# Kernel optimization log

Hardware: AMD Instinct MI355X
Metric: run time of the kernel (lower is better)

## Reference

```python
import math
import jax, jax.numpy as jnp
import numpy as np

BATCH, DEPTH = 16, 12
N_NODES = 2 ** DEPTH - 1  # 4095, heap layout: children of i are 2i+1, 2i+2
IN_F, OUT_F, STATE_F = 512, 512, 256


def setup_inputs() -> dict:
    key = jax.random.key(0)
    ks = jax.random.split(key, 10)
    x_batch = jax.random.normal(ks[0], (BATCH, N_NODES, IN_F), dtype=jnp.float32)
    idx_batch = jnp.arange(BATCH, dtype=jnp.int32)
    W_in = jax.random.normal(ks[1], (IN_F, IN_F), dtype=jnp.float32) / math.sqrt(IN_F)
    b_in = jnp.zeros((IN_F,), dtype=jnp.float32)
    u1 = jax.random.uniform(ks[2], (STATE_F,), dtype=jnp.float32)
    u2 = jax.random.uniform(ks[3], (STATE_F,), dtype=jnp.float32)
    nu_log = jnp.log(-0.5 * jnp.log(u1 + 1e-6))
    theta_log = jnp.log(2.0 * math.pi * u2)
    lam_mod = jnp.exp(-jnp.exp(nu_log))
    gamma_log = jnp.log(jnp.sqrt(1.0 - jnp.square(lam_mod)))
    B_re = jax.random.normal(ks[4], (STATE_F, IN_F), dtype=jnp.float32) / math.sqrt(2 * IN_F)
    B_im = jax.random.normal(ks[5], (STATE_F, IN_F), dtype=jnp.float32) / math.sqrt(2 * IN_F)
    C_re = jax.random.normal(ks[6], (OUT_F, STATE_F), dtype=jnp.float32) / math.sqrt(STATE_F)
    C_im = jax.random.normal(ks[7], (OUT_F, STATE_F), dtype=jnp.float32) / math.sqrt(STATE_F)
    return dict(x_batch=x_batch, idx_batch=idx_batch, W_in=W_in, b_in=b_in,
                nu_log=nu_log, theta_log=theta_log, gamma_log=gamma_log,
                B_re=B_re, B_im=B_im, C_re=C_re, C_im=C_im)


def reference(x_batch, idx_batch, W_in, b_in, nu_log, theta_log, gamma_log,
              B_re, B_im, C_re, C_im):
    bsz, n_nodes, _ = x_batch.shape
    depth = int(round(math.log2(n_nodes + 1)))
    S = B_re.shape[0]

    # LRU constants (complex lambda kept as (re, im) pair)
    lam_mod = jnp.exp(-jnp.exp(nu_log))           # [S]
    th = jnp.exp(theta_log)
    lr, li = lam_mod * jnp.cos(th), lam_mod * jnp.sin(th)
    gamma = jnp.exp(gamma_log)                    # [S]

    proj = x_batch @ W_in.T + b_in                # [B, N, IN]
    # complex input term (proj is real): proj @ B^T
    in_re = jnp.einsum('bni,si->bns', proj, B_re) # [B, N, S]
    in_im = jnp.einsum('bni,si->bns', proj, B_im)

    h_re = jnp.zeros((bsz, n_nodes, S), dtype=proj.dtype)
    h_im = jnp.zeros((bsz, n_nodes, S), dtype=proj.dtype)

    # process levels bottom-up; level d nodes occupy [2^d-1, 2^{d+1}-1)
    for d in range(depth - 1, -1, -1):
        a, b = 2 ** d - 1, 2 ** (d + 1) - 1
        n = b - a
        if d == depth - 1:  # leaves: left/right = -1 -> zero child state
            cr = jnp.zeros((bsz, n, S), dtype=proj.dtype)
            ci = jnp.zeros((bsz, n, S), dtype=proj.dtype)
        else:
            # children of nodes [a, b) are the contiguous block [2a+1, 2b+1)
            cr = h_re[:, 2 * a + 1:2 * b + 1].reshape(bsz, n, 2, S).sum(axis=2)
            ci = h_im[:, 2 * a + 1:2 * b + 1].reshape(bsz, n, 2, S).sum(axis=2)
        hr = lr * cr - li * ci + gamma * in_re[:, a:b]
        hi = lr * ci + li * cr + gamma * in_im[:, a:b]
        h_re = h_re.at[:, a:b].set(hr)
        h_im = h_im.at[:, a:b].set(hi)

    # y = Re(h @ C^T), computed once on final states (same math as per-level scatter)
    outputs = jnp.einsum('bns,os->bno', h_re, C_re) - jnp.einsum('bns,os->bno', h_im, C_im)
    return outputs
```

## Files before the change

kernel.cpp:

```cpp
#include <hip/hip_runtime.h>


#define ROWS 65520
#define KDIM 512

typedef __attribute__((ext_vector_type(8))) short bf16x8;
typedef __attribute__((ext_vector_type(4))) float f32x4;

__device__ __forceinline__ unsigned short f2bf(float f) {
    unsigned int u = __float_as_uint(f);
    unsigned int r = (u + 0x7FFFu + ((u >> 16) & 1u)) >> 16;
    return (unsigned short)r;
}
__device__ __forceinline__ float b2f(unsigned short h) {
    return __uint_as_float(((unsigned int)h) << 16);
}

__global__ __launch_bounds__(256) void cvt_f32_bf16(const float* __restrict__ in,
                                                    unsigned short* __restrict__ out,
                                                    int n4) {
    int i = blockIdx.x * 256 + threadIdx.x;
    if (i < n4) {
        float4 v = ((const float4*)in)[i];
        ushort4 o;
        o.x = f2bf(v.x); o.y = f2bf(v.y); o.z = f2bf(v.z); o.w = f2bf(v.w);
        ((ushort4*)out)[i] = o;
    }
}

__global__ __launch_bounds__(256) void prep_M(const float* __restrict__ W,
                                              const float* __restrict__ Bre,
                                              const float* __restrict__ Bim,
                                              const float* __restrict__ gamma_log,
                                              unsigned short* __restrict__ M16) {
    __shared__ float Bs[16][17];
    __shared__ float Ws[16][17];
    int tx = threadIdx.x, ty = threadIdx.y;
    int j  = blockIdx.x * 16 + tx;
    int cc = blockIdx.y * 16 + ty;
    const float* Bsel = (cc < 256) ? (Bre + (size_t)cc * 512)
                                   : (Bim + (size_t)(cc - 256) * 512);
    float acc = 0.f;
    for (int kt = 0; kt < 512; kt += 16) {
        Bs[ty][tx] = Bsel[kt + tx];
        Ws[ty][tx] = W[(size_t)(kt + ty) * 512 + j];
        __syncthreads();
#pragma unroll
        for (int k = 0; k < 16; ++k) acc += Bs[ty][k] * Ws[k][tx];
        __syncthreads();
    }
    float g = expf(gamma_log[cc & 255]);
    M16[(size_t)cc * 512 + j] = f2bf(acc * g);
}

__global__ __launch_bounds__(64) void prep_bias(const float* __restrict__ bin,
                                                const float* __restrict__ Bre,
                                                const float* __restrict__ Bim,
                                                const float* __restrict__ gamma_log,
                                                float* __restrict__ biasc) {
    const int c = blockIdx.x;
    const int t = threadIdx.x;
    const float* Bsel = (c < 256) ? (Bre + (size_t)c * 512)
                                  : (Bim + (size_t)(c - 256) * 512);
    float acc = 0.f;
#pragma unroll
    for (int i = t; i < 512; i += 64) acc += bin[i] * Bsel[i];
#pragma unroll
    for (int off = 32; off > 0; off >>= 1) acc += __shfl_down(acc, off, 64);
    if (t == 0) biasc[c] = acc * expf(gamma_log[c & 255]);
}

__global__ __launch_bounds__(256) void prep_C(const float* __restrict__ Cre,
                                              const float* __restrict__ Cim,
                                              unsigned short* __restrict__ C16) {
    int idx = blockIdx.x * 256 + threadIdx.x;
    int o = idx >> 9;
    int s = idx & 511;
    float v = (s < 256) ? Cre[(size_t)o * 256 + s] : -Cim[(size_t)o * 256 + (s - 256)];
    C16[idx] = f2bf(v);
}

template <bool OUT_BF16>
__global__ __launch_bounds__(256) void gemm_mfma(const unsigned short* __restrict__ A,
                                                 const unsigned short* __restrict__ Bm,
                                                 const float* __restrict__ bias,
                                                 void* __restrict__ Cout,
                                                 int Mrows) {
    __shared__ __align__(16) unsigned short As[128 * 64];
    __shared__ __align__(16) unsigned short Bs[128 * 64];
    const int t = threadIdx.x;
    const int lane = t & 63;
    const int w = t >> 6;
    const int wr = (w >> 1) * 64;
    const int wc = (w & 1) * 64;
    const int bid = blockIdx.x;
    const int xcd = bid & 7;
    const int lid = bid >> 3;
    const int rowblk = xcd * 64 + (lid >> 2);
    const int colblk = lid & 3;
    const int row0 = rowblk * 128;
    const int col0 = colblk * 128;
    const int kt0  = (rowblk & 7) * 64;

    f32x4 acc[4][4] = {};

    for (int it = 0; it < 8; ++it) {
        const int kt = (kt0 + it * 64) & 511;
#pragma unroll
        for (int q = 0; q < 4; ++q) {
            int c   = q * 256 + t;
            int row = c >> 3;
            int kc  = c & 7;
            int kg  = kc ^ (row & 7);
            int ar  = row0 + row; if (ar >= Mrows) ar = Mrows - 1;
            const unsigned short* ga = A + (size_t)ar * KDIM + kt + kg * 8;
            __builtin_amdgcn_global_load_lds(
                (const __attribute__((address_space(1))) unsigned int*)ga,
                (__attribute__((address_space(3))) unsigned int*)(As + c * 8),
                16, 0, 0);
            const unsigned short* gb = Bm + (size_t)(col0 + row) * KDIM + kt + kg * 8;
            __builtin_amdgcn_global_load_lds(
                (const __attribute__((address_space(1))) unsigned int*)gb,
                (__attribute__((address_space(3))) unsigned int*)(Bs + c * 8),
                16, 0, 0);
        }
        __syncthreads();
#pragma unroll
        for (int kk = 0; kk < 64; kk += 32) {
            const int kgc = kk >> 3;
            bf16x8 af[4], bfr[4];
#pragma unroll
            for (int i = 0; i < 4; ++i) {
                int row = wr + i * 16 + (lane & 15);
                int kca = (kgc + (lane >> 4)) ^ (row & 7);
                af[i] = *(const bf16x8*)(As + row * 64 + kca * 8);
                int colr = wc + i * 16 + (lane & 15);
                int kcb = (kgc + (lane >> 4)) ^ (colr & 7);
                bfr[i] = *(const bf16x8*)(Bs + colr * 64 + kcb * 8);
            }
#pragma unroll
            for (int i = 0; i < 4; ++i)
#pragma unroll
                for (int j = 0; j < 4; ++j)
                    acc[i][j] = __builtin_amdgcn_mfma_f32_16x16x32_bf16(
                        af[i], bfr[j], acc[i][j], 0, 0, 0);
        }
        __syncthreads();
    }

    const int cq = lane >> 4;
    const int cl = lane & 15;
#pragma unroll
    for (int i = 0; i < 4; ++i) {
#pragma unroll
        for (int j = 0; j < 4; ++j) {
#pragma unroll
            for (int r = 0; r < 4; ++r) {
                int grow = row0 + wr + i * 16 + cq * 4 + r;
                int gcol = col0 + wc + j * 16 + cl;
                if (grow < Mrows) {
                    float v = acc[i][j][r];
                    if (bias) v += bias[gcol];
                    if (OUT_BF16)
                        ((unsigned short*)Cout)[(size_t)grow * 512 + gcol] = f2bf(v);
                    else
                        ((float*)Cout)[(size_t)grow * 512 + gcol] = v;
                }
            }
        }
    }
}

template <int E>
__global__ __launch_bounds__(256) void tree_up(unsigned short* __restrict__ buf,
                                               const float* __restrict__ nu_log,
                                               const float* __restrict__ theta_log,
                                               int root_base) {
    const int b = blockIdx.x;
    const int rs = root_base + blockIdx.y;
    const int c = threadIdx.x;
    constexpr int LEAVES = 1 << E;
    const float lam = expf(-expf(nu_log[c]));
    const float th  = expf(theta_log[c]);
    const float lr  = lam * cosf(th);
    const float li  = lam * sinf(th);
    const size_t base = (size_t)b * 4095;

    float vr[LEAVES], vi[LEAVES];
    {
        const int nbL = ((rs + 1) << E) - 1;
#pragma unroll
        for (int i = 0; i < LEAVES; ++i) {
            const size_t r = (base + nbL + i) * 512;
            vr[i] = b2f(buf[r + c]);
            vi[i] = b2f(buf[r + 256 + c]);
        }
    }
    float gr[LEAVES - 1], gi[LEAVES - 1];
    {
        int idx = 0;
#pragma unroll
        for (int e = E - 1; e >= 0; --e) {
            const int n  = 1 << e;
            const int nb = ((rs + 1) << e) - 1;
#pragma unroll
            for (int i = 0; i < n; ++i) {
                const size_t r = (base + nb + i) * 512;
                gr[idx] = b2f(buf[r + c]);
                gi[idx] = b2f(buf[r + 256 + c]);
                ++idx;
            }
        }
    }
    {
        int idx = 0;
#pragma unroll
        for (int e = E - 1; e >= 0; --e) {
            const int n  = 1 << e;
            const int nb = ((rs + 1) << e) - 1;
#pragma unroll
            for (int i = 0; i < n; ++i) {
                const float cr = vr[2 * i] + vr[2 * i + 1];
                const float ci = vi[2 * i] + vi[2 * i + 1];
                const float hr = lr * cr - li * ci + gr[idx];
                const float hi = lr * ci + li * cr + gi[idx];
                ++idx;
                const size_t r = (base + nb + i) * 512;
                buf[r + c]       = f2bf(hr);
                buf[r + 256 + c] = f2bf(hi);
                vr[i] = hr;
                vi[i] = hi;
            }
        }
    }
}

extern "C" void kernel_launch(void* const* d_in, const int* in_sizes, int n_in,
                              void* d_out, int out_size, void* d_ws, size_t ws_size,
                              hipStream_t stream) {
    const float* x         = (const float*)d_in[0];
    const float* W_in      = (const float*)d_in[2];
    const float* b_in      = (const float*)d_in[3];
    const float* nu_log    = (const float*)d_in[4];
    const float* theta_log = (const float*)d_in[5];
    const float* gamma_log = (const float*)d_in[6];
    const float* B_re      = (const float*)d_in[7];
    const float* B_im      = (const float*)d_in[8];
    const float* C_re      = (const float*)d_in[9];
    const float* C_im      = (const float*)d_in[10];
    float* out = (float*)d_out;

    char* ws = (char*)d_ws;
    const size_t HB = (size_t)ROWS * 512 * 2;
    unsigned short* x16   = (unsigned short*)ws;
    unsigned short* hb16  = (unsigned short*)(ws + HB);
    unsigned short* M16   = (unsigned short*)(ws + 2 * HB);
    unsigned short* C16   = (unsigned short*)(ws + 2 * HB + 512 * 512 * 2);
    float*          biasc = (float*)(ws + 2 * HB + 2 * 512 * 512 * 2);

    const int n4 = ROWS * 512 / 4;
    cvt_f32_bf16<<<(n4 + 255) / 256, 256, 0, stream>>>(x, x16, n4);
    prep_M<<<dim3(32, 32), dim3(16, 16), 0, stream>>>(W_in, B_re, B_im, gamma_log, M16);
    prep_bias<<<512, 64, 0, stream>>>(b_in, B_re, B_im, gamma_log, biasc);
    prep_C<<<1024, 256, 0, stream>>>(C_re, C_im, C16);

    gemm_mfma<true><<<2048, 256, 0, stream>>>(x16, M16, biasc, hb16, ROWS);

    tree_up<4><<<dim3(16, 128), 256, 0, stream>>>(hb16, nu_log, theta_log, 127);
    tree_up<4><<<dim3(16, 8),   256, 0, stream>>>(hb16, nu_log, theta_log, 7);
    tree_up<3><<<dim3(16, 1),   256, 0, stream>>>(hb16, nu_log, theta_log, 0);

    gemm_mfma<false><<<2048, 256, 0, stream>>>(hb16, C16, nullptr, out, ROWS);
}
```

Before: 422.5 us.

## Double-buffer GEMM LDS tiles and merge prep kernels into one launch

The MFMA GEMM now keeps two LDS buffers and issues the async global-to-LDS loads for the next K tile before computing on the current one, so load latency can overlap with MFMA work. The four small preparation kernels (x conversion, fused W·B matrix, bias, C packing) are merged into a single launch that dispatches on block index, saving launch gaps. Doubling LDS to 64KB per block may reduce occupancy. The single remaining barrier per iteration may also not order the async loads correctly with respect to buffer reuse.

```diff
diff --git a/kernel.cpp b/kernel.cpp
--- a/kernel.cpp
+++ b/kernel.cpp
@@ -16,68 +16,74 @@
     return __uint_as_float(((unsigned int)h) << 16);
 }
 
-__global__ __launch_bounds__(256) void cvt_f32_bf16(const float* __restrict__ in,
-                                                    unsigned short* __restrict__ out,
-                                                    int n4) {
-    int i = blockIdx.x * 256 + threadIdx.x;
-    if (i < n4) {
-        float4 v = ((const float4*)in)[i];
-        ushort4 o;
-        o.x = f2bf(v.x); o.y = f2bf(v.y); o.z = f2bf(v.z); o.w = f2bf(v.w);
-        ((ushort4*)out)[i] = o;
-    }
-}
-
-__global__ __launch_bounds__(256) void prep_M(const float* __restrict__ W,
-                                              const float* __restrict__ Bre,
-                                              const float* __restrict__ Bim,
-                                              const float* __restrict__ gamma_log,
-                                              unsigned short* __restrict__ M16) {
-    __shared__ float Bs[16][17];
-    __shared__ float Ws[16][17];
-    int tx = threadIdx.x, ty = threadIdx.y;
-    int j  = blockIdx.x * 16 + tx;
-    int cc = blockIdx.y * 16 + ty;
-    const float* Bsel = (cc < 256) ? (Bre + (size_t)cc * 512)
-                                   : (Bim + (size_t)(cc - 256) * 512);
-    float acc = 0.f;
-    for (int kt = 0; kt < 512; kt += 16) {
-        Bs[ty][tx] = Bsel[kt + tx];
-        Ws[ty][tx] = W[(size_t)(kt + ty) * 512 + j];
-        __syncthreads();
-#pragma unroll
-        for (int k = 0; k < 16; ++k) acc += Bs[ty][k] * Ws[k][tx];
-        __syncthreads();
-    }
-    float g = expf(gamma_log[cc & 255]);
-    M16[(size_t)cc * 512 + j] = f2bf(acc * g);
-}
-
-__global__ __launch_bounds__(64) void prep_bias(const float* __restrict__ bin,
+#define CVT_BLKS  32760
+#define PM_BASE   32760
+#define PC_BASE   33784
+#define PB_BASE   34808
+#define PREP_GRID 34936
+
+__global__ __launch_bounds__(256) void prep_all(const float* __restrict__ x,
+                                                unsigned short* __restrict__ x16,
+                                                const float* __restrict__ W,
                                                 const float* __restrict__ Bre,
                                                 const float* __restrict__ Bim,
                                                 const float* __restrict__ gamma_log,
-                                                float* __restrict__ biasc) {
-    const int c = blockIdx.x;
+                                                unsigned short* __restrict__ M16,
+                                                const float* __restrict__ bin,
+                                                float* __restrict__ biasc,
+                                                const float* __restrict__ Cre,
+                                                const float* __restrict__ Cim,
+                                                unsigned short* __restrict__ C16) {
+    __shared__ float Bs[16][17];
+    __shared__ float Ws[16][17];
+    const int blk = blockIdx.x;
     const int t = threadIdx.x;
-    const float* Bsel = (c < 256) ? (Bre + (size_t)c * 512)
-                                  : (Bim + (size_t)(c - 256) * 512);
-    float acc = 0.f;
-#pragma unroll
-    for (int i = t; i < 512; i += 64) acc += bin[i] * Bsel[i];
-#pragma unroll
-    for (int off = 32; off > 0; off >>= 1) acc += __shfl_down(acc, off, 64);
-    if (t == 0) biasc[c] = acc * expf(gamma_log[c & 255]);
-}
-
-__global__ __launch_bounds__(256) void prep_C(const float* __restrict__ Cre,
-                                              const float* __restrict__ Cim,
-                                              unsigned short* __restrict__ C16) {
-    int idx = blockIdx.x * 256 + threadIdx.x;
-    int o = idx >> 9;
-    int s = idx & 511;
-    float v = (s < 256) ? Cre[(size_t)o * 256 + s] : -Cim[(size_t)o * 256 + (s - 256)];
-    C16[idx] = f2bf(v);
+
+    if (blk < CVT_BLKS) {
+        int i = blk * 256 + t;
+        float4 v = ((const float4*)x)[i];
+        ushort4 o;
+        o.x = f2bf(v.x); o.y = f2bf(v.y); o.z = f2bf(v.z); o.w = f2bf(v.w);
+        ((ushort4*)x16)[i] = o;
+    } else if (blk < PC_BASE) {
+        const int pm = blk - PM_BASE;
+        const int bx = pm & 31;
+        const int by = pm >> 5;
+        const int tx = t & 15;
+        const int ty = t >> 4;
+        const int j  = bx * 16 + tx;
+        const int cc = by * 16 + ty;
+        const float* Bsel = (cc < 256) ? (Bre + (size_t)cc * 512)
+                                       : (Bim + (size_t)(cc - 256) * 512);
+        float acc = 0.f;
+        for (int kt = 0; kt < 512; kt += 16) {
+            Bs[ty][tx] = Bsel[kt + tx];
+            Ws[ty][tx] = W[(size_t)(kt + ty) * 512 + j];
+            __syncthreads();
+#pragma unroll
+            for (int k = 0; k < 16; ++k) acc += Bs[ty][k] * Ws[k][tx];
+            __syncthreads();
+        }
+        float g = expf(gamma_log[cc & 255]);
+        M16[(size_t)cc * 512 + j] = f2bf(acc * g);
+    } else if (blk < PB_BASE) {
+        int idx = (blk - PC_BASE) * 256 + t;
+        int o = idx >> 9;
+        int s = idx & 511;
+        float v = (s < 256) ? Cre[(size_t)o * 256 + s] : -Cim[(size_t)o * 256 + (s - 256)];
+        C16[idx] = f2bf(v);
+    } else {
+        const int c = (blk - PB_BASE) * 4 + (t >> 6);
+        const int lane = t & 63;
+        const float* Bsel = (c < 256) ? (Bre + (size_t)c * 512)
+                                      : (Bim + (size_t)(c - 256) * 512);
+        float acc = 0.f;
+#pragma unroll
+        for (int i = lane; i < 512; i += 64) acc += bin[i] * Bsel[i];
+#pragma unroll
+        for (int off = 32; off > 0; off >>= 1) acc += __shfl_down(acc, off, 64);
+        if (lane == 0) biasc[c] = acc * expf(gamma_log[c & 255]);
+    }
 }
 
 template <bool OUT_BF16>
@@ -86,8 +92,8 @@
                                                  const float* __restrict__ bias,
                                                  void* __restrict__ Cout,
                                                  int Mrows) {
-    __shared__ __align__(16) unsigned short As[128 * 64];
-    __shared__ __align__(16) unsigned short Bs[128 * 64];
+    __shared__ __align__(16) unsigned short As[2][128 * 64];
+    __shared__ __align__(16) unsigned short Bs[2][128 * 64];
     const int t = threadIdx.x;
     const int lane = t & 63;
     const int w = t >> 6;
@@ -104,27 +110,35 @@
 
     f32x4 acc[4][4] = {};
 
+#define STAGE(pb, itv)                                                         \
+    do {                                                                       \
+        const int kt_ = (kt0 + (itv) * 64) & 511;                              \
+        _Pragma("unroll")                                                      \
+        for (int q = 0; q < 4; ++q) {                                          \
+            int c_   = q * 256 + t;                                            \
+            int row_ = c_ >> 3;                                                \
+            int kc_  = c_ & 7;                                                 \
+            int kg_  = kc_ ^ (row_ & 7);                                       \
+            int ar_  = row0 + row_; if (ar_ >= Mrows) ar_ = Mrows - 1;         \
+            const unsigned short* ga_ = A + (size_t)ar_ * KDIM + kt_ + kg_ * 8;\
+            __builtin_amdgcn_global_load_lds(                                  \
+                (const __attribute__((address_space(1))) unsigned int*)ga_,    \
+                (__attribute__((address_space(3))) unsigned int*)(&As[pb][c_ * 8]),\
+                16, 0, 0);                                                     \
+            const unsigned short* gb_ = Bm + (size_t)(col0 + row_) * KDIM + kt_ + kg_ * 8;\
+            __builtin_amdgcn_global_load_lds(                                  \
+                (const __attribute__((address_space(1))) unsigned int*)gb_,    \
+                (__attribute__((address_space(3))) unsigned int*)(&Bs[pb][c_ * 8]),\
+                16, 0, 0);                                                     \
+        }                                                                      \
+    } while (0)
+
+    STAGE(0, 0);
+    __syncthreads();
+
+    int cur = 0;
     for (int it = 0; it < 8; ++it) {
-        const int kt = (kt0 + it * 64) & 511;
-#pragma unroll
-        for (int q = 0; q < 4; ++q) {
-            int c   = q * 256 + t;
-            int row = c >> 3;
-            int kc  = c & 7;
-            int kg  = kc ^ (row & 7);
-            int ar  = row0 + row; if (ar >= Mrows) ar = Mrows - 1;
-            const unsigned short* ga = A + (size_t)ar * KDIM + kt + kg * 8;
-            __builtin_amdgcn_global_load_lds(
-                (const __attribute__((address_space(1))) unsigned int*)ga,
-                (__attribute__((address_space(3))) unsigned int*)(As + c * 8),
-                16, 0, 0);
-            const unsigned short* gb = Bm + (size_t)(col0 + row) * KDIM + kt + kg * 8;
-            __builtin_amdgcn_global_load_lds(
-                (const __attribute__((address_space(1))) unsigned int*)gb,
-                (__attribute__((address_space(3))) unsigned int*)(Bs + c * 8),
-                16, 0, 0);
-        }
-        __syncthreads();
+        if (it < 7) STAGE(cur ^ 1, it + 1);
 #pragma unroll
         for (int kk = 0; kk < 64; kk += 32) {
             const int kgc = kk >> 3;
@@ -133,10 +147,10 @@
             for (int i = 0; i < 4; ++i) {
                 int row = wr + i * 16 + (lane & 15);
                 int kca = (kgc + (lane >> 4)) ^ (row & 7);
-                af[i] = *(const bf16x8*)(As + row * 64 + kca * 8);
+                af[i] = *(const bf16x8*)(&As[cur][row * 64 + kca * 8]);
                 int colr = wc + i * 16 + (lane & 15);
                 int kcb = (kgc + (lane >> 4)) ^ (colr & 7);
-                bfr[i] = *(const bf16x8*)(Bs + colr * 64 + kcb * 8);
+                bfr[i] = *(const bf16x8*)(&Bs[cur][colr * 64 + kcb * 8]);
             }
 #pragma unroll
             for (int i = 0; i < 4; ++i)
@@ -146,7 +160,9 @@
                         af[i], bfr[j], acc[i][j], 0, 0, 0);
         }
         __syncthreads();
-    }
+        cur ^= 1;
+    }
+#undef STAGE
 
     const int cq = lane >> 4;
     const int cl = lane & 15;
@@ -258,11 +274,8 @@
     unsigned short* C16   = (unsigned short*)(ws + 2 * HB + 512 * 512 * 2);
     float*          biasc = (float*)(ws + 2 * HB + 2 * 512 * 512 * 2);
 
-    const int n4 = ROWS * 512 / 4;
-    cvt_f32_bf16<<<(n4 + 255) / 256, 256, 0, stream>>>(x, x16, n4);
-    prep_M<<<dim3(32, 32), dim3(16, 16), 0, stream>>>(W_in, B_re, B_im, gamma_log, M16);
-    prep_bias<<<512, 64, 0, stream>>>(b_in, B_re, B_im, gamma_log, biasc);
-    prep_C<<<1024, 256, 0, stream>>>(C_re, C_im, C16);
+    prep_all<<<PREP_GRID, 256, 0, stream>>>(x, x16, W_in, B_re, B_im, gamma_log,
+                                            M16, b_in, biasc, C_re, C_im, C16);
 
     gemm_mfma<true><<<2048, 256, 0, stream>>>(x16, M16, biasc, hb16, ROWS);
 
```

Result: faster. 413.5 us (-2.1%).
